# Kernel optimization log

Measured on AMD Instinct MI355X. Metric: run time of the kernel, lower is better.

## Reference

```python
import jax, jax.numpy as jnp
import numpy as np

N, E = 50000, 800000
C_IN, C_OUT, HID = 64, 64, 64


def setup_inputs() -> dict:
    key = jax.random.key(0)
    ks = jax.random.split(key, 12)
    def rn(k, shape, scale=0.05):
        return jax.random.normal(k, shape, dtype=jnp.float32) * scale
    return dict(
        x=jax.random.normal(ks[0], (N, C_IN), dtype=jnp.float32),
        pos=jax.random.normal(ks[1], (N, 3), dtype=jnp.float32),
        edge_index=jax.random.randint(ks[2], (2, E), 0, N),
        W_in=rn(ks[3], (C_IN, C_IN)), b_in=jnp.zeros((C_IN,), jnp.float32),
        W_out=rn(ks[4], (C_OUT, C_OUT)), b_out=jnp.zeros((C_OUT,), jnp.float32),
        W_lin=rn(ks[5], (C_OUT, C_IN)),   # PointTransformerConv.lin (value), bias=False
        W_src=rn(ks[6], (C_OUT, C_IN)),   # lin_src, bias=False
        W_dst=rn(ks[7], (C_OUT, C_IN)),   # lin_dst, bias=False
        pos_w1=rn(ks[8], (HID, 3)), pos_b1=jnp.zeros((HID,), jnp.float32),
        pos_w2=rn(ks[9], (C_OUT, HID)), pos_b2=jnp.zeros((C_OUT,), jnp.float32),
        att_w1=rn(ks[10], (HID, C_OUT)), att_b1=jnp.zeros((HID,), jnp.float32),
        att_w2=rn(ks[11], (C_OUT, HID)), att_b2=jnp.zeros((C_OUT,), jnp.float32),
    )


def _mlp2(y, w1, b1, w2, b2):
    # MLP([a, 64, b], batch_norm=False): Linear->ReLU->Linear->ReLU
    y = jax.nn.relu(y @ w1.T + b1)
    return jax.nn.relu(y @ w2.T + b2)


def reference(x, pos, edge_index, W_in, b_in, W_out, b_out, W_lin, W_src, W_dst,
              pos_w1, pos_b1, pos_w2, pos_b2, att_w1, att_b1, att_w2, att_b2):
    n = x.shape[0]
    h = jax.nn.relu(x @ W_in.T + b_in)            # lin_in + relu, (N, C_in)
    v = h @ W_lin.T                                # value projection (N, C_out)
    k_src = h @ W_src.T                            # alpha_j source part
    q_dst = h @ W_dst.T                            # alpha_i dest part
    # PointTransformerConv adds self-loops by default
    loop = jnp.arange(n)
    src = jnp.concatenate([edge_index[0], loop])   # (E+N,)
    dst = jnp.concatenate([edge_index[1], loop])
    # per-edge positional encoding: pos_nn(pos_i - pos_j)
    delta = _mlp2(pos[dst] - pos[src], pos_w1, pos_b1, pos_w2, pos_b2)
    # per-edge attention logits: attn_nn(alpha_i - alpha_j), (E+N, C_out)
    alpha = _mlp2(q_dst[dst] - k_src[src], att_w1, att_b1, att_w2, att_b2)
    # per-destination-node channelwise softmax (self-loops ensure no empty segment)
    amax = jax.ops.segment_max(alpha, dst, num_segments=n)
    ex = jnp.exp(alpha - amax[dst])
    denom = jax.ops.segment_sum(ex, dst, num_segments=n)
    w = ex / (denom[dst] + 1e-16)
    # message = alpha * (x_j + delta); aggregate = sum over neighbors
    out = jax.ops.segment_sum(w * (v[src] + delta), dst, num_segments=n)
    return jax.nn.relu(out @ W_out.T + b_out)
```

## Files before the change

### kernel.cpp

```cpp
#include <hip/hip_runtime.h>
#include <math.h>

#define NN 50000
#define EE 800000
#define ET (EE + NN)
#define C  64
#define NBLK 49
#define NCHUNK 831
#define ZBLK 463

typedef __attribute__((ext_vector_type(8))) _Float16 f16x8;
typedef __attribute__((ext_vector_type(4))) _Float16 f16x4;
typedef __attribute__((ext_vector_type(2))) _Float16 f16x2;
typedef __attribute__((ext_vector_type(4))) float f32x4;

__device__ __forceinline__ f16x2 pk2(float a, float b) {
  return __builtin_bit_cast(f16x2, __builtin_amdgcn_cvt_pkrtz(a, b));
}
__device__ __forceinline__ f16x4 pk4(float a, float b, float c, float d) {
  return __builtin_shufflevector(pk2(a, b), pk2(c, d), 0, 1, 2, 3);
}
__device__ __forceinline__ f16x8 pk8(const float* y) {
  const f16x4 lo = pk4(y[0], y[1], y[2], y[3]);
  const f16x4 hi = pk4(y[4], y[5], y[6], y[7]);
  return __builtin_shufflevector(lo, hi, 0, 1, 2, 3, 4, 5, 6, 7);
}

__device__ __forceinline__ f16x8 frag_ldh(const _Float16* base, int row,
                                          int kofs) {
  return *(const f16x8*)(base + row * 72 + kofs);
}

__device__ __forceinline__ void stage_w(_Float16* __restrict__ dst,
                                        const _Float16* __restrict__ src16,
                                        int tid) {
  const f16x8* src = (const f16x8*)(src16 + tid * 16);
  _Float16* d = dst + (tid >> 2) * 72 + (tid & 3) * 16;
  ((f16x8*)d)[0] = src[0];
  ((f16x8*)d)[1] = src[1];
}

__device__ __forceinline__ int psl(int e, int o) {
  return (e + 2 * o + (o >> 5)) & 63;
}

__global__ __launch_bounds__(256) void prep_kernel(
    const float* __restrict__ W_in, const float* __restrict__ W_lin,
    const float* __restrict__ W_src, const float* __restrict__ W_dst,
    const float* __restrict__ att_w1, const float* __restrict__ att_w2,
    const float* __restrict__ pos_w2, const float* __restrict__ W_out,
    _Float16* __restrict__ w16, int* __restrict__ cnt2) {
  const float* Ws[8] = {W_in, W_lin, W_src, W_dst, att_w1, att_w2, pos_w2, W_out};
  const float* src = Ws[blockIdx.x];
  _Float16* dst = w16 + blockIdx.x * 4096;
#pragma unroll
  for (int i = threadIdx.x * 4; i < 4096; i += 1024) {
    const float4 w = *(const float4*)(src + i);
    *(f16x4*)(dst + i) = pk4(w.x, w.y, w.z, w.w);
  }
  int4* cz = (int4*)(cnt2 + blockIdx.x * NN);
#pragma unroll 1
  for (int i = threadIdx.x; i < NN / 4; i += 256) cz[i] = make_int4(0, 0, 0, 0);
}

__global__ __launch_bounds__(256) void scan_partial(const int* __restrict__ cnt2,
                                                    int* __restrict__ bsum,
                                                    float* __restrict__ zeroreg) {
  const int t = threadIdx.x;
  if (blockIdx.x >= NBLK) {
    const int zb = blockIdx.x - NBLK;
    float4* dst = (float4*)zeroreg;
    const int total4 = 2 * NN * 64 / 4;
    const float4 z = make_float4(0.f, 0.f, 0.f, 0.f);
#pragma unroll 1
    for (int i = zb * 256 + t; i < total4; i += ZBLK * 256) dst[i] = z;
    return;
  }
  __shared__ int ws[4];
  const int base = blockIdx.x * 1024 + t * 4;
  int s = 0;
  if (base + 3 < NN) {
#pragma unroll
    for (int sh = 0; sh < 8; ++sh) {
      const int4 v = *(const int4*)(cnt2 + sh * NN + base);
      s += v.x + v.y + v.z + v.w;
    }
  } else {
#pragma unroll
    for (int i = 0; i < 4; ++i)
      if (base + i < NN)
#pragma unroll
        for (int sh = 0; sh < 8; ++sh) s += cnt2[sh * NN + base + i];
  }
#pragma unroll
  for (int off = 32; off; off >>= 1) s += __shfl_down(s, off, 64);
  if ((t & 63) == 0) ws[t >> 6] = s;
  __syncthreads();
  if (t == 0) bsum[blockIdx.x] = ws[0] + ws[1] + ws[2] + ws[3];
}

__global__ __launch_bounds__(256) void scan_final(const int* __restrict__ cnt2,
                                                  const int* __restrict__ bsum,
                                                  int* __restrict__ curs2) {
  __shared__ int tsum[256];
  __shared__ int sblk[64];
  const int t = threadIdx.x;
  if (t < 64) {
    const int mine = (t < NBLK) ? bsum[t] : 0;
    int v = mine;
#pragma unroll
    for (int off = 1; off < 64; off <<= 1) {
      const int u = __shfl_up(v, off, 64);
      if (t >= off) v += u;
    }
    sblk[t] = v - mine;
  }
  const int base = blockIdx.x * 1024 + t * 4;
  int c2[8][4];
  int v[4] = {0, 0, 0, 0};
  if (base + 3 < NN) {
#pragma unroll
    for (int sh = 0; sh < 8; ++sh) {
      const int4 x = *(const int4*)(cnt2 + sh * NN + base);
      c2[sh][0] = x.x; c2[sh][1] = x.y; c2[sh][2] = x.z; c2[sh][3] = x.w;
      v[0] += x.x; v[1] += x.y; v[2] += x.z; v[3] += x.w;
    }
  } else {
#pragma unroll
    for (int sh = 0; sh < 8; ++sh)
#pragma unroll
      for (int i = 0; i < 4; ++i) {
        const int c = (base + i < NN) ? cnt2[sh * NN + base + i] : 0;
        c2[sh][i] = c;
        v[i] += c;
      }
  }
  const int s = v[0] + v[1] + v[2] + v[3];
  tsum[t] = s;
  __syncthreads();
  for (int off = 1; off < 256; off <<= 1) {
    const int u = (t >= off) ? tsum[t - off] : 0;
    __syncthreads();
    tsum[t] += u;
    __syncthreads();
  }
  int ex = sblk[blockIdx.x] + tsum[t] - s;
  int offs[8][4];
#pragma unroll
  for (int i = 0; i < 4; ++i) {
    int run = ex;
#pragma unroll
    for (int sh = 0; sh < 8; ++sh) {
      offs[sh][i] = run;
      run += c2[sh][i];
    }
    ex += v[i];
  }
  if (base + 3 < NN) {
#pragma unroll
    for (int sh = 0; sh < 8; ++sh)
      *(int4*)(curs2 + sh * NN + base) =
          make_int4(offs[sh][0], offs[sh][1], offs[sh][2], offs[sh][3]);
  } else {
#pragma unroll
    for (int sh = 0; sh < 8; ++sh)
#pragma unroll
      for (int i = 0; i < 4; ++i)
        if (base + i < NN) curs2[sh * NN + base + i] = offs[sh][i];
  }
}

__global__ __launch_bounds__(256) void scatter_kernel(const int* __restrict__ ei,
                                                      int* __restrict__ curs2,
                                                      int2* __restrict__ srt) {
  const int chunk = blockIdx.x;
  int* cs = curs2 + (chunk & 7) * NN;
  const int e0 = chunk * 1024 + threadIdx.x * 4;
  if (e0 >= ET) return;
  int s[4], d[4];
  if (e0 + 3 < EE) {
    const int4 sv = *(const int4*)(ei + e0);
    const int4 dv = *(const int4*)(ei + EE + e0);
    s[0] = sv.x; s[1] = sv.y; s[2] = sv.z; s[3] = sv.w;
    d[0] = dv.x; d[1] = dv.y; d[2] = dv.z; d[3] = dv.w;
  } else {
#pragma unroll
    for (int i = 0; i < 4; ++i) {
      const int e = e0 + i;
      if (e < EE) {
        s[i] = ei[e];
        d[i] = ei[EE + e];
      } else if (e < ET) {
        s[i] = d[i] = e - EE;
      } else {
        s[i] = d[i] = -1;
      }
    }
  }
#pragma unroll
  for (int i = 0; i < 4; ++i) {
    if (d[i] >= 0) {
      const int p = atomicAdd(&cs[d[i]], 1);
      srt[p] = make_int2(s[i], d[i]);
    }
  }
}

__global__ __launch_bounds__(256, 3) void node_proj(
    const float* __restrict__ x, const float* __restrict__ b_in,
    const _Float16* __restrict__ w16, const int* __restrict__ ei,
    int* __restrict__ cnt2, _Float16* __restrict__ vh,
    _Float16* __restrict__ kh, _Float16* __restrict__ qh) {
  __shared__ __align__(16) _Float16 wlds[4 * 4608];
  __shared__ __align__(16) _Float16 hlds[4608];
  __shared__ float biasv[64];

  const int tid = threadIdx.x;
  const int nb = blockIdx.x * 64;
  const int l15 = tid & 15;
  const int quad = (tid >> 4) & 3;
  const int wband = tid >> 6;
  const int nloc = wband * 16 + l15;
  const int gn = nb + nloc;

#pragma unroll 1
  for (int chunk = blockIdx.x; chunk < NCHUNK; chunk += gridDim.x) {
    int* cs = cnt2 + (chunk & 7) * NN;
    const int e0 = chunk * 1024 + tid * 4;
    if (e0 < ET) {
      int d[4];
      if (e0 + 3 < EE) {
        const int4 dv = *(const int4*)(ei + EE + e0);
        d[0] = dv.x; d[1] = dv.y; d[2] = dv.z; d[3] = dv.w;
      } else {
#pragma unroll
        for (int i = 0; i < 4; ++i) {
          const int e = e0 + i;
          d[i] = (e < EE) ? ei[EE + e] : ((e < ET) ? e - EE : -1);
        }
      }
#pragma unroll
      for (int i = 0; i < 4; ++i)
        if (d[i] >= 0) atomicAdd(&cs[d[i]], 1);
    }
  }

#pragma unroll
  for (int w = 0; w < 4; ++w) stage_w(wlds + w * 4608, w16 + w * 4096, tid);
  if (tid < 64) biasv[tid] = b_in[tid];

  f16x8 bfrag[2];
#pragma unroll
  for (int ks = 0; ks < 2; ++ks) {
    float y[8] = {0.f, 0.f, 0.f, 0.f, 0.f, 0.f, 0.f, 0.f};
    if (gn < NN) {
      const float4 a = *(const float4*)(x + (size_t)gn * 64 + ks * 32 + quad * 8);
      const float4 b = *(const float4*)(x + (size_t)gn * 64 + ks * 32 + quad * 8 + 4);
      y[0] = a.x; y[1] = a.y; y[2] = a.z; y[3] = a.w;
      y[4] = b.x; y[5] = b.y; y[6] = b.z; y[7] = b.w;
    }
    bfrag[ks] = pk8(y);
  }
  __syncthreads();

#pragma unroll
  for (int t = 0; t < 4; ++t) {
    f32x4 acc = {0.f, 0.f, 0.f, 0.f};
#pragma unroll
    for (int ks = 0; ks < 2; ++ks) {
      const f16x8 af = frag_ldh(wlds, t * 16 + l15, ks * 32 + quad * 8);
      acc = __builtin_amdgcn_mfma_f32_16x16x32_f16(af, bfrag[ks], acc, 0, 0, 0);
    }
    const int hb = t * 16 + quad * 4;
    *(f16x4*)(hlds + nloc * 72 + hb) =
        pk4(fmaxf(acc[0] + biasv[hb + 0], 0.f), fmaxf(acc[1] + biasv[hb + 1], 0.f),
            fmaxf(acc[2] + biasv[hb + 2], 0.f), fmaxf(acc[3] + biasv[hb + 3], 0.f));
  }
  __syncthreads();

  f16x8 hfrag[2];
#pragma unroll
  for (int ks = 0; ks < 2; ++ks)
    hfrag[ks] = frag_ldh(hlds, nloc, ks * 32 + quad * 8);

  _Float16* outs[3] = {vh, kh, qh};
#pragma unroll
  for (int p = 0; p < 3; ++p) {
    const _Float16* W = wlds + (p + 1) * 4608;
#pragma unroll
    for (int t = 0; t < 4; ++t) {
      f32x4 acc = {0.f, 0.f, 0.f, 0.f};
#pragma unroll
      for (int ks = 0; ks < 2; ++ks) {
        const f16x8 af = frag_ldh(W, t * 16 + l15, ks * 32 + quad * 8);
        acc = __builtin_amdgcn_mfma_f32_16x16x32_f16(af, hfrag[ks], acc, 0, 0, 0);
      }
      if (gn < NN) {
        *(f16x4*)(outs[p] + (size_t)gn * 64 + t * 16 + quad * 4) =
            pk4(acc[0], acc[1], acc[2], acc[3]);
      }
    }
  }
}

__global__ __launch_bounds__(256, 5) void edge_pass(
    const int2* __restrict__ srt, const float* __restrict__ pos,
    const _Float16* __restrict__ vh, const _Float16* __restrict__ kh,
    const _Float16* __restrict__ qh, const _Float16* __restrict__ w16,
    const float* __restrict__ att_b1, const float* __restrict__ att_b2,
    const float* __restrict__ pos_w1, const float* __restrict__ pos_b1,
    const float* __restrict__ pos_b2, float* __restrict__ num,
    float* __restrict__ den) {
  __shared__ __align__(16) _Float16 smem[13824];
  __shared__ __align__(16) float posw1T[3 * 64];
  __shared__ float b1s[64], b2s[64], pb1s[64], pb2s[64];
  __shared__ int dsts[64];

  _Float16* W1 = smem;
  _Float16* W2 = smem + 4608;
  _Float16* HP = smem + 9216;
  f16x2* pairb = (f16x2*)smem;

  const int tid = threadIdx.x;
  const int eb = blockIdx.x * 64;
  const int l15 = tid & 15;
  const int quad = (tid >> 4) & 3;
  const int wband = tid >> 6;
  const int eloc = wband * 16 + l15;

  int s_mine, d_mine;
  f16x8 bfrag[2];
  float dp0, dp1, dp2;
  {
    const int e = eb + eloc;
    int2 sd = make_int2(0, 0);
    int valid_d = -1;
    if (e < ET) {
      sd = srt[e];
      valid_d = sd.y;
    }
    s_mine = sd.x;
    d_mine = sd.y;
    if (quad == 0) dsts[eloc] = valid_d;
#pragma unroll
    for (int ks = 0; ks < 2; ++ks) {
      const f16x8 qv =
          *(const f16x8*)(qh + (size_t)d_mine * 64 + ks * 32 + quad * 8);
      const f16x8 kv =
          *(const f16x8*)(kh + (size_t)s_mine * 64 + ks * 32 + quad * 8);
      bfrag[ks] = qv - kv;
    }
    dp0 = pos[(size_t)d_mine * 3 + 0] - pos[(size_t)s_mine * 3 + 0];
    dp1 = pos[(size_t)d_mine * 3 + 1] - pos[(size_t)s_mine * 3 + 1];
    dp2 = pos[(size_t)d_mine * 3 + 2] - pos[(size_t)s_mine * 3 + 2];
  }

  stage_w(W1, w16 + 4 * 4096, tid);
  stage_w(W2, w16 + 5 * 4096, tid);
  if (tid < 64) {
    b1s[tid] = att_b1[tid];
    b2s[tid] = att_b2[tid];
    pb1s[tid] = pos_b1[tid];
    pb2s[tid] = pos_b2[tid];
    posw1T[0 * 64 + tid] = pos_w1[tid * 3 + 0];
    posw1T[1 * 64 + tid] = pos_w1[tid * 3 + 1];
    posw1T[2 * 64 + tid] = pos_w1[tid * 3 + 2];
  }
  __syncthreads();

#pragma unroll
  for (int t = 0; t < 4; ++t) {
    f32x4 acc = {0.f, 0.f, 0.f, 0.f};
#pragma unroll
    for (int ks = 0; ks < 2; ++ks) {
      const f16x8 af = frag_ldh(W1, t * 16 + l15, ks * 32 + quad * 8);
      acc = __builtin_amdgcn_mfma_f32_16x16x32_f16(af, bfrag[ks], acc, 0, 0, 0);
    }
    const int hb = t * 16 + quad * 4;
    *(f16x4*)(HP + eloc * 72 + hb) =
        pk4(fmaxf(acc[0] + b1s[hb + 0], 0.f), fmaxf(acc[1] + b1s[hb + 1], 0.f),
            fmaxf(acc[2] + b1s[hb + 2], 0.f), fmaxf(acc[3] + b1s[hb + 3], 0.f));
  }

  f16x8 hpfrag[2];
#pragma unroll
  for (int ks = 0; ks < 2; ++ks) {
    float hv[8];
#pragma unroll
    for (int j = 0; j < 8; ++j) {
      const int i = ks * 32 + quad * 8 + j;
      float h = pb1s[i];
      h = fmaf(dp0, posw1T[i], h);
      h = fmaf(dp1, posw1T[64 + i], h);
      h = fmaf(dp2, posw1T[128 + i], h);
      hv[j] = fmaxf(h, 0.f);
    }
    hpfrag[ks] = pk8(hv);
  }

  float ex[16];
  {
    f16x8 hfrag[2];
#pragma unroll
    for (int ks = 0; ks < 2; ++ks)
      hfrag[ks] = frag_ldh(HP, eloc, ks * 32 + quad * 8);
#pragma unroll
    for (int t = 0; t < 4; ++t) {
      f32x4 acc = {0.f, 0.f, 0.f, 0.f};
#pragma unroll
      for (int ks = 0; ks < 2; ++ks) {
        const f16x8 af = frag_ldh(W2, t * 16 + l15, ks * 32 + quad * 8);
        acc = __builtin_amdgcn_mfma_f32_16x16x32_f16(af, hfrag[ks], acc, 0, 0, 0);
      }
      const int ob = t * 16 + quad * 4;
#pragma unroll
      for (int r = 0; r < 4; ++r)
        ex[t * 4 + r] = __expf(fmaxf(acc[r] + b2s[ob + r], 0.f));
    }
  }
  float vr[16];
#pragma unroll
  for (int t = 0; t < 4; ++t) {
    const f16x4 v4 = *(const f16x4*)(vh + (size_t)s_mine * 64 + t * 16 + quad * 4);
    vr[t * 4 + 0] = (float)v4[0];
    vr[t * 4 + 1] = (float)v4[1];
    vr[t * 4 + 2] = (float)v4[2];
    vr[t * 4 + 3] = (float)v4[3];
  }
  __syncthreads();

  stage_w(HP, w16 + 6 * 4096, tid);
  __syncthreads();

  float del[16];
#pragma unroll
  for (int t = 0; t < 4; ++t) {
    f32x4 acc = {0.f, 0.f, 0.f, 0.f};
#pragma unroll
    for (int ks = 0; ks < 2; ++ks) {
      const f16x8 af = frag_ldh(HP, t * 16 + l15, ks * 32 + quad * 8);
      acc = __builtin_amdgcn_mfma_f32_16x16x32_f16(af, hpfrag[ks], acc, 0, 0, 0);
    }
    const int ob = t * 16 + quad * 4;
#pragma unroll
    for (int r = 0; r < 4; ++r)
      del[t * 4 + r] = fmaxf(acc[r] + pb2s[ob + r], 0.f);
  }

#pragma unroll
  for (int t = 0; t < 4; ++t) {
#pragma unroll
    for (int r = 0; r < 4; ++r) {
      const int o = t * 16 + quad * 4 + r;
      const float e_ = ex[t * 4 + r];
      pairb[o * 64 + psl(eloc, o)] =
          pk2(e_ * (vr[t * 4 + r] + del[t * 4 + r]), e_);
    }
  }
  __syncthreads();

  {
    const int c = tid & 63;
    const int r = tid >> 6;
    float am = 0.f, ae = 0.f;
    int cur = -1;
#pragma unroll 1
    for (int t2 = 0; t2 < 16; ++t2) {
      const int el = r * 16 + t2;
      const int d = dsts[el];
      if (d != cur) {
        if (cur >= 0) {
          unsafeAtomicAdd(num + (size_t)cur * 64 + c, am);
          unsafeAtomicAdd(den + (size_t)cur * 64 + c, ae);
        }
        cur = d;
        am = 0.f;
        ae = 0.f;
      }
      if (d >= 0) {
        const f16x2 pe = pairb[c * 64 + psl(el, c)];
        am += (float)pe[0];
        ae += (float)pe[1];
      }
    }
    if (cur >= 0) {
      unsafeAtomicAdd(num + (size_t)cur * 64 + c, am);
      unsafeAtomicAdd(den + (size_t)cur * 64 + c, ae);
    }
  }
}

__global__ __launch_bounds__(256, 4) void out_proj(
    const float* __restrict__ num, const float* __restrict__ den,
    const _Float16* __restrict__ w16, const float* __restrict__ b_out,
    float* __restrict__ out) {
  __shared__ __align__(16) _Float16 wlds[4608];
  __shared__ float biasv[64];

  const int tid = threadIdx.x;
  const int nb = blockIdx.x * 64;
  const int l15 = tid & 15;
  const int quad = (tid >> 4) & 3;
  const int wband = tid >> 6;
  const int gn = nb + wband * 16 + l15;

  stage_w(wlds, w16 + 7 * 4096, tid);
  if (tid < 64) biasv[tid] = b_out[tid];

  f16x8 bfrag[2];
#pragma unroll
  for (int ks = 0; ks < 2; ++ks) {
    float y[8] = {0.f, 0.f, 0.f, 0.f, 0.f, 0.f, 0.f, 0.f};
    if (gn < NN) {
      const size_t base = (size_t)gn * 64 + ks * 32 + quad * 8;
      const float4 n0 = *(const float4*)(num + base);
      const float4 n1 = *(const float4*)(num + base + 4);
      const float4 d0 = *(const float4*)(den + base);
      const float4 d1 = *(const float4*)(den + base + 4);
      y[0] = n0.x / (d0.x + 1e-16f); y[1] = n0.y / (d0.y + 1e-16f);
      y[2] = n0.z / (d0.z + 1e-16f); y[3] = n0.w / (d0.w + 1e-16f);
      y[4] = n1.x / (d1.x + 1e-16f); y[5] = n1.y / (d1.y + 1e-16f);
      y[6] = n1.z / (d1.z + 1e-16f); y[7] = n1.w / (d1.w + 1e-16f);
    }
    bfrag[ks] = pk8(y);
  }
  __syncthreads();

#pragma unroll
  for (int t = 0; t < 4; ++t) {
    f32x4 acc = {0.f, 0.f, 0.f, 0.f};
#pragma unroll
    for (int ks = 0; ks < 2; ++ks) {
      const f16x8 af = frag_ldh(wlds, t * 16 + l15, ks * 32 + quad * 8);
      acc = __builtin_amdgcn_mfma_f32_16x16x32_f16(af, bfrag[ks], acc, 0, 0, 0);
    }
    if (gn < NN) {
      const int ob = t * 16 + quad * 4;
      float4 r;
      r.x = fmaxf(acc[0] + biasv[ob + 0], 0.f);
      r.y = fmaxf(acc[1] + biasv[ob + 1], 0.f);
      r.z = fmaxf(acc[2] + biasv[ob + 2], 0.f);
      r.w = fmaxf(acc[3] + biasv[ob + 3], 0.f);
      *(float4*)(out + (size_t)gn * 64 + ob) = r;
    }
  }
}

extern "C" void kernel_launch(void* const* d_in, const int* in_sizes, int n_in,
                              void* d_out, int out_size, void* d_ws,
                              size_t ws_size, hipStream_t stream) {
  const float* x      = (const float*)d_in[0];
  const float* pos    = (const float*)d_in[1];
  const int*   ei     = (const int*)d_in[2];
  const float* W_in   = (const float*)d_in[3];
  const float* b_in   = (const float*)d_in[4];
  const float* W_out  = (const float*)d_in[5];
  const float* b_out  = (const float*)d_in[6];
  const float* W_lin  = (const float*)d_in[7];
  const float* W_src  = (const float*)d_in[8];
  const float* W_dst  = (const float*)d_in[9];
  const float* pos_w1 = (const float*)d_in[10];
  const float* pos_b1 = (const float*)d_in[11];
  const float* pos_w2 = (const float*)d_in[12];
  const float* pos_b2 = (const float*)d_in[13];
  const float* att_w1 = (const float*)d_in[14];
  const float* att_b1 = (const float*)d_in[15];
  const float* att_w2 = (const float*)d_in[16];
  const float* att_b2 = (const float*)d_in[17];

  float* ws = (float*)d_ws;
  const size_t NC = (size_t)NN * C;
  float* num = ws;
  float* den = ws + NC;
  _Float16* vh = (_Float16*)(ws + 2 * NC);
  _Float16* kh = vh + NC;
  _Float16* qh = kh + NC;
  _Float16* w16 = qh + NC;
  int* ib     = (int*)(w16 + 8 * 4096);
  int* cnt2   = ib;
  int* curs2  = ib + 8 * NN;
  int* bsum   = ib + 16 * NN;
  int2* srt   = (int2*)(((uintptr_t)(bsum + NBLK) + 15) & ~(uintptr_t)15);

  const dim3 blk(256);
  prep_kernel<<<dim3(8), blk, 0, stream>>>(W_in, W_lin, W_src, W_dst, att_w1,
                                           att_w2, pos_w2, W_out, w16, cnt2);
  node_proj<<<dim3((NN + 63) / 64), blk, 0, stream>>>(x, b_in, w16, ei, cnt2,
                                                      vh, kh, qh);
  scan_partial<<<dim3(NBLK + ZBLK), blk, 0, stream>>>(cnt2, bsum, num);
  scan_final<<<dim3(NBLK), blk, 0, stream>>>(cnt2, bsum, curs2);
  scatter_kernel<<<dim3(NCHUNK), blk, 0, stream>>>(ei, curs2, srt);
  edge_pass<<<dim3((ET + 63) / 64), blk, 0, stream>>>(
      srt, pos, vh, kh, qh, w16, att_b1, att_b2, pos_w1, pos_b1, pos_b2, num,
      den);
  out_proj<<<dim3((NN + 63) / 64), blk, 0, stream>>>(num, den, w16, b_out,
                                                     (float*)d_out);
}
```

Measured before the change: 300.5 us.

## Reduce per-destination edge segments with MFMA selection matrices instead of scalar loops

The per-block segmented reduction of (weighted message, exp) pairs now runs as MFMA matrix multiplies against a 0/1 selection matrix. That matrix is built from a ballot over destination-run boundaries and handles up to 8 runs per pass, then each run is written with atomic adds. The softmax exponent switches to exp2, with log2(e) folded into the fp16 att_w2 weights and the att_b2 bias. The prep kernel is widened to 64 blocks for zeroing the count buffer. The cost is extra LDS staging and syncs, and a loop whose trip count depends on how many runs a block has. The fp16 rounding of the scaled weights changes numerics slightly.

```diff
diff --git a/kernel.cpp b/kernel.cpp
--- a/kernel.cpp
+++ b/kernel.cpp
@@ -40,27 +40,28 @@
   ((f16x8*)d)[1] = src[1];
 }
 
-__device__ __forceinline__ int psl(int e, int o) {
-  return (e + 2 * o + (o >> 5)) & 63;
-}
-
 __global__ __launch_bounds__(256) void prep_kernel(
     const float* __restrict__ W_in, const float* __restrict__ W_lin,
     const float* __restrict__ W_src, const float* __restrict__ W_dst,
     const float* __restrict__ att_w1, const float* __restrict__ att_w2,
     const float* __restrict__ pos_w2, const float* __restrict__ W_out,
     _Float16* __restrict__ w16, int* __restrict__ cnt2) {
-  const float* Ws[8] = {W_in, W_lin, W_src, W_dst, att_w1, att_w2, pos_w2, W_out};
-  const float* src = Ws[blockIdx.x];
-  _Float16* dst = w16 + blockIdx.x * 4096;
-#pragma unroll
-  for (int i = threadIdx.x * 4; i < 4096; i += 1024) {
-    const float4 w = *(const float4*)(src + i);
-    *(f16x4*)(dst + i) = pk4(w.x, w.y, w.z, w.w);
-  }
-  int4* cz = (int4*)(cnt2 + blockIdx.x * NN);
+  if (blockIdx.x < 8) {
+    const float* Ws[8] = {W_in, W_lin, W_src, W_dst, att_w1, att_w2, pos_w2,
+                          W_out};
+    const float* src = Ws[blockIdx.x];
+    _Float16* dst = w16 + blockIdx.x * 4096;
+    const float sc = (blockIdx.x == 5) ? 1.44269504088896340736f : 1.0f;
+#pragma unroll
+    for (int i = threadIdx.x * 4; i < 4096; i += 1024) {
+      const float4 w = *(const float4*)(src + i);
+      *(f16x4*)(dst + i) = pk4(w.x * sc, w.y * sc, w.z * sc, w.w * sc);
+    }
+  }
+  int4* cz = (int4*)cnt2;
 #pragma unroll 1
-  for (int i = threadIdx.x; i < NN / 4; i += 256) cz[i] = make_int4(0, 0, 0, 0);
+  for (int i = blockIdx.x * 256 + threadIdx.x; i < 2 * NN; i += 64 * 256)
+    cz[i] = make_int4(0, 0, 0, 0);
 }
 
 __global__ __launch_bounds__(256) void scan_partial(const int* __restrict__ cnt2,
@@ -315,17 +316,20 @@
   __shared__ __align__(16) float posw1T[3 * 64];
   __shared__ float b1s[64], b2s[64], pb1s[64], pb2s[64];
   __shared__ int dsts[64];
+  __shared__ int dstu[64];
 
   _Float16* W1 = smem;
   _Float16* W2 = smem + 4608;
   _Float16* HP = smem + 9216;
-  f16x2* pairb = (f16x2*)smem;
+  _Float16* PAIR = smem;
+  _Float16* ST = smem + 9216;
 
   const int tid = threadIdx.x;
   const int eb = blockIdx.x * 64;
   const int l15 = tid & 15;
   const int quad = (tid >> 4) & 3;
   const int wband = tid >> 6;
+  const int lane = tid & 63;
   const int eloc = wband * 16 + l15;
 
   int s_mine, d_mine;
@@ -359,7 +363,7 @@
   stage_w(W2, w16 + 5 * 4096, tid);
   if (tid < 64) {
     b1s[tid] = att_b1[tid];
-    b2s[tid] = att_b2[tid];
+    b2s[tid] = att_b2[tid] * 1.44269504088896340736f;
     pb1s[tid] = pos_b1[tid];
     pb2s[tid] = pos_b2[tid];
     posw1T[0 * 64 + tid] = pos_w1[tid * 3 + 0];
@@ -367,6 +371,17 @@
     posw1T[2 * 64 + tid] = pos_w1[tid * 3 + 2];
   }
   __syncthreads();
+
+  int rid_self, R, dball;
+  {
+    dball = dsts[lane];
+    const int dprev = dsts[(lane > 0) ? (lane - 1) : 0];
+    const bool flag = (dball >= 0) && (lane == 0 || dball != dprev);
+    const unsigned long long m = __ballot(flag);
+    R = (int)__popcll(m);
+    rid_self = (int)__popcll(m & ((2ull << lane) - 1)) - 1;
+    if (wband == 0 && flag) dstu[rid_self] = dball;
+  }
 
 #pragma unroll
   for (int t = 0; t < 4; ++t) {
@@ -415,7 +430,7 @@
       const int ob = t * 16 + quad * 4;
 #pragma unroll
       for (int r = 0; r < 4; ++r)
-        ex[t * 4 + r] = __expf(fmaxf(acc[r] + b2s[ob + r], 0.f));
+        ex[t * 4 + r] = __builtin_exp2f(fmaxf(acc[r] + b2s[ob + r], 0.f));
     }
   }
   float vr[16];
@@ -453,40 +468,57 @@
     for (int r = 0; r < 4; ++r) {
       const int o = t * 16 + quad * 4 + r;
       const float e_ = ex[t * 4 + r];
-      pairb[o * 64 + psl(eloc, o)] =
+      *(f16x2*)(PAIR + o * 136 + eloc * 2) =
           pk2(e_ * (vr[t * 4 + r] + del[t * 4 + r]), e_);
     }
   }
   __syncthreads();
 
-  {
-    const int c = tid & 63;
-    const int r = tid >> 6;
-    float am = 0.f, ae = 0.f;
-    int cur = -1;
+  if (wband == 0) {
+    const f16x8 z = {0, 0, 0, 0, 0, 0, 0, 0};
 #pragma unroll 1
-    for (int t2 = 0; t2 < 16; ++t2) {
-      const int el = r * 16 + t2;
-      const int d = dsts[el];
-      if (d != cur) {
-        if (cur >= 0) {
-          unsafeAtomicAdd(num + (size_t)cur * 64 + c, am);
-          unsafeAtomicAdd(den + (size_t)cur * 64 + c, ae);
-        }
-        cur = d;
-        am = 0.f;
-        ae = 0.f;
+    for (int i = lane; i < 272; i += 64) ((f16x8*)ST)[i] = z;
+    if (dball >= 0 && rid_self < 8) {
+      ST[(2 * rid_self + 0) * 136 + 2 * lane + 0] = (_Float16)1.0f;
+      ST[(2 * rid_self + 1) * 136 + 2 * lane + 1] = (_Float16)1.0f;
+    }
+  }
+  __syncthreads();
+
+  const int chq = wband * 16 + quad * 4;
+  const int jrun = l15 >> 1;
+  float* const base_np = (l15 & 1) ? den : num;
+#pragma unroll 1
+  for (int rt = 0;; ++rt) {
+    f32x4 racc = {0.f, 0.f, 0.f, 0.f};
+#pragma unroll
+    for (int ks = 0; ks < 4; ++ks) {
+      const f16x8 af =
+          *(const f16x8*)(PAIR + (wband * 16 + l15) * 136 + ks * 32 + quad * 8);
+      const f16x8 bf = *(const f16x8*)(ST + l15 * 136 + ks * 32 + quad * 8);
+      racc = __builtin_amdgcn_mfma_f32_16x16x32_f16(af, bf, racc, 0, 0, 0);
+    }
+    const int run = rt * 8 + jrun;
+    if (run < R) {
+      float* p = base_np + (size_t)dstu[run] * 64 + chq;
+      unsafeAtomicAdd(p + 0, racc[0]);
+      unsafeAtomicAdd(p + 1, racc[1]);
+      unsafeAtomicAdd(p + 2, racc[2]);
+      unsafeAtomicAdd(p + 3, racc[3]);
+    }
+    if ((rt + 1) * 8 >= R) break;
+    __syncthreads();
+    if (wband == 0) {
+      const f16x8 z = {0, 0, 0, 0, 0, 0, 0, 0};
+#pragma unroll 1
+      for (int i = lane; i < 272; i += 64) ((f16x8*)ST)[i] = z;
+      const int lr = rid_self - (rt + 1) * 8;
+      if (dball >= 0 && lr >= 0 && lr < 8) {
+        ST[(2 * lr + 0) * 136 + 2 * lane + 0] = (_Float16)1.0f;
+        ST[(2 * lr + 1) * 136 + 2 * lane + 1] = (_Float16)1.0f;
       }
-      if (d >= 0) {
-        const f16x2 pe = pairb[c * 64 + psl(el, c)];
-        am += (float)pe[0];
-        ae += (float)pe[1];
-      }
-    }
-    if (cur >= 0) {
-      unsafeAtomicAdd(num + (size_t)cur * 64 + c, am);
-      unsafeAtomicAdd(den + (size_t)cur * 64 + c, ae);
-    }
+    }
+    __syncthreads();
   }
 }
 
@@ -583,8 +615,8 @@
   int2* srt   = (int2*)(((uintptr_t)(bsum + NBLK) + 15) & ~(uintptr_t)15);
 
   const dim3 blk(256);
-  prep_kernel<<<dim3(8), blk, 0, stream>>>(W_in, W_lin, W_src, W_dst, att_w1,
-                                           att_w2, pos_w2, W_out, w16, cnt2);
+  prep_kernel<<<dim3(64), blk, 0, stream>>>(W_in, W_lin, W_src, W_dst, att_w1,
+                                            att_w2, pos_w2, W_out, w16, cnt2);
   node_proj<<<dim3((NN + 63) / 64), blk, 0, stream>>>(x, b_in, w16, ei, cnt2,
                                                       vh, kh, qh);
   scan_partial<<<dim3(NBLK + ZBLK), blk, 0, stream>>>(cnt2, bsum, num);
```

Result: slower. 337.1 us (+12.2%).

## Swizzle edge-pass LDS weight tiles, use exp2 with folded log2e, widen prep grid

Applied to the files above, without the earlier changes.

The padded 72-stride LDS layout for the attention and positional MLP weights and the hidden tile is replaced by an unpadded 128-byte-row XOR swizzle. This cuts shared memory per block so occupancy can go from 5 to 6 blocks per CU while still avoiding bank conflicts. log2(e) is folded into att_w2 during prep and into att_b2 at load, so the softmax uses exp2 instead of expf; since ReLU commutes with a positive scale this gives the same result. The prep kernel now runs on 64 blocks instead of 8 to spread out zeroing the count arrays. The risk is higher register pressure from the tighter launch bound.

```diff
diff --git a/kernel.cpp b/kernel.cpp
--- a/kernel.cpp
+++ b/kernel.cpp
@@ -30,7 +30,6 @@
                                           int kofs) {
   return *(const f16x8*)(base + row * 72 + kofs);
 }
-
 __device__ __forceinline__ void stage_w(_Float16* __restrict__ dst,
                                         const _Float16* __restrict__ src16,
                                         int tid) {
@@ -40,6 +39,23 @@
   ((f16x8*)d)[1] = src[1];
 }
 
+__device__ __forceinline__ int swzb(int row, int colbyte) {
+  return row * 128 + (colbyte ^ ((row & 7) << 4));
+}
+__device__ __forceinline__ f16x8 frag_lds(const _Float16* base, int row,
+                                          int kofs) {
+  return *(const f16x8*)((const char*)base + swzb(row, kofs * 2));
+}
+__device__ __forceinline__ void stage_ws(_Float16* __restrict__ dst,
+                                         const _Float16* __restrict__ src16,
+                                         int tid) {
+  const f16x8* src = (const f16x8*)(src16 + tid * 16);
+  const int row = tid >> 2;
+  const int c0 = (tid & 3) * 32;
+  *(f16x8*)((char*)dst + swzb(row, c0)) = src[0];
+  *(f16x8*)((char*)dst + swzb(row, c0 + 16)) = src[1];
+}
+
 __device__ __forceinline__ int psl(int e, int o) {
   return (e + 2 * o + (o >> 5)) & 63;
 }
@@ -50,17 +66,22 @@
     const float* __restrict__ att_w1, const float* __restrict__ att_w2,
     const float* __restrict__ pos_w2, const float* __restrict__ W_out,
     _Float16* __restrict__ w16, int* __restrict__ cnt2) {
-  const float* Ws[8] = {W_in, W_lin, W_src, W_dst, att_w1, att_w2, pos_w2, W_out};
-  const float* src = Ws[blockIdx.x];
-  _Float16* dst = w16 + blockIdx.x * 4096;
-#pragma unroll
-  for (int i = threadIdx.x * 4; i < 4096; i += 1024) {
-    const float4 w = *(const float4*)(src + i);
-    *(f16x4*)(dst + i) = pk4(w.x, w.y, w.z, w.w);
-  }
-  int4* cz = (int4*)(cnt2 + blockIdx.x * NN);
+  if (blockIdx.x < 8) {
+    const float* Ws[8] = {W_in, W_lin, W_src, W_dst, att_w1, att_w2, pos_w2,
+                          W_out};
+    const float* src = Ws[blockIdx.x];
+    _Float16* dst = w16 + blockIdx.x * 4096;
+    const float sc = (blockIdx.x == 5) ? 1.44269504088896340736f : 1.0f;
+#pragma unroll
+    for (int i = threadIdx.x * 4; i < 4096; i += 1024) {
+      const float4 w = *(const float4*)(src + i);
+      *(f16x4*)(dst + i) = pk4(w.x * sc, w.y * sc, w.z * sc, w.w * sc);
+    }
+  }
+  int4* cz = (int4*)cnt2;
 #pragma unroll 1
-  for (int i = threadIdx.x; i < NN / 4; i += 256) cz[i] = make_int4(0, 0, 0, 0);
+  for (int i = blockIdx.x * 256 + threadIdx.x; i < 2 * NN; i += 64 * 256)
+    cz[i] = make_int4(0, 0, 0, 0);
 }
 
 __global__ __launch_bounds__(256) void scan_partial(const int* __restrict__ cnt2,
@@ -303,7 +324,7 @@
   }
 }
 
-__global__ __launch_bounds__(256, 5) void edge_pass(
+__global__ __launch_bounds__(256, 6) void edge_pass(
     const int2* __restrict__ srt, const float* __restrict__ pos,
     const _Float16* __restrict__ vh, const _Float16* __restrict__ kh,
     const _Float16* __restrict__ qh, const _Float16* __restrict__ w16,
@@ -311,14 +332,14 @@
     const float* __restrict__ pos_w1, const float* __restrict__ pos_b1,
     const float* __restrict__ pos_b2, float* __restrict__ num,
     float* __restrict__ den) {
-  __shared__ __align__(16) _Float16 smem[13824];
+  __shared__ __align__(16) _Float16 smem[12288];
   __shared__ __align__(16) float posw1T[3 * 64];
   __shared__ float b1s[64], b2s[64], pb1s[64], pb2s[64];
   __shared__ int dsts[64];
 
   _Float16* W1 = smem;
-  _Float16* W2 = smem + 4608;
-  _Float16* HP = smem + 9216;
+  _Float16* W2 = smem + 4096;
+  _Float16* HP = smem + 8192;
   f16x2* pairb = (f16x2*)smem;
 
   const int tid = threadIdx.x;
@@ -355,11 +376,11 @@
     dp2 = pos[(size_t)d_mine * 3 + 2] - pos[(size_t)s_mine * 3 + 2];
   }
 
-  stage_w(W1, w16 + 4 * 4096, tid);
-  stage_w(W2, w16 + 5 * 4096, tid);
+  stage_ws(W1, w16 + 4 * 4096, tid);
+  stage_ws(W2, w16 + 5 * 4096, tid);
   if (tid < 64) {
     b1s[tid] = att_b1[tid];
-    b2s[tid] = att_b2[tid];
+    b2s[tid] = att_b2[tid] * 1.44269504088896340736f;
     pb1s[tid] = pos_b1[tid];
     pb2s[tid] = pos_b2[tid];
     posw1T[0 * 64 + tid] = pos_w1[tid * 3 + 0];
@@ -373,11 +394,11 @@
     f32x4 acc = {0.f, 0.f, 0.f, 0.f};
 #pragma unroll
     for (int ks = 0; ks < 2; ++ks) {
-      const f16x8 af = frag_ldh(W1, t * 16 + l15, ks * 32 + quad * 8);
+      const f16x8 af = frag_lds(W1, t * 16 + l15, ks * 32 + quad * 8);
       acc = __builtin_amdgcn_mfma_f32_16x16x32_f16(af, bfrag[ks], acc, 0, 0, 0);
     }
     const int hb = t * 16 + quad * 4;
-    *(f16x4*)(HP + eloc * 72 + hb) =
+    *(f16x4*)((char*)HP + swzb(eloc, hb * 2)) =
         pk4(fmaxf(acc[0] + b1s[hb + 0], 0.f), fmaxf(acc[1] + b1s[hb + 1], 0.f),
             fmaxf(acc[2] + b1s[hb + 2], 0.f), fmaxf(acc[3] + b1s[hb + 3], 0.f));
   }
@@ -403,19 +424,19 @@
     f16x8 hfrag[2];
 #pragma unroll
     for (int ks = 0; ks < 2; ++ks)
-      hfrag[ks] = frag_ldh(HP, eloc, ks * 32 + quad * 8);
+      hfrag[ks] = frag_lds(HP, eloc, ks * 32 + quad * 8);
 #pragma unroll
     for (int t = 0; t < 4; ++t) {
       f32x4 acc = {0.f, 0.f, 0.f, 0.f};
 #pragma unroll
       for (int ks = 0; ks < 2; ++ks) {
-        const f16x8 af = frag_ldh(W2, t * 16 + l15, ks * 32 + quad * 8);
+        const f16x8 af = frag_lds(W2, t * 16 + l15, ks * 32 + quad * 8);
         acc = __builtin_amdgcn_mfma_f32_16x16x32_f16(af, hfrag[ks], acc, 0, 0, 0);
       }
       const int ob = t * 16 + quad * 4;
 #pragma unroll
       for (int r = 0; r < 4; ++r)
-        ex[t * 4 + r] = __expf(fmaxf(acc[r] + b2s[ob + r], 0.f));
+        ex[t * 4 + r] = __builtin_exp2f(fmaxf(acc[r] + b2s[ob + r], 0.f));
     }
   }
   float vr[16];
@@ -429,7 +450,7 @@
   }
   __syncthreads();
 
-  stage_w(HP, w16 + 6 * 4096, tid);
+  stage_ws(HP, w16 + 6 * 4096, tid);
   __syncthreads();
 
   float del[16];
@@ -438,7 +459,7 @@
     f32x4 acc = {0.f, 0.f, 0.f, 0.f};
 #pragma unroll
     for (int ks = 0; ks < 2; ++ks) {
-      const f16x8 af = frag_ldh(HP, t * 16 + l15, ks * 32 + quad * 8);
+      const f16x8 af = frag_lds(HP, t * 16 + l15, ks * 32 + quad * 8);
       acc = __builtin_amdgcn_mfma_f32_16x16x32_f16(af, hpfrag[ks], acc, 0, 0, 0);
     }
     const int ob = t * 16 + quad * 4;
@@ -583,8 +604,8 @@
   int2* srt   = (int2*)(((uintptr_t)(bsum + NBLK) + 15) & ~(uintptr_t)15);
 
   const dim3 blk(256);
-  prep_kernel<<<dim3(8), blk, 0, stream>>>(W_in, W_lin, W_src, W_dst, att_w1,
-                                           att_w2, pos_w2, W_out, w16, cnt2);
+  prep_kernel<<<dim3(64), blk, 0, stream>>>(W_in, W_lin, W_src, W_dst, att_w1,
+                                            att_w2, pos_w2, W_out, w16, cnt2);
   node_proj<<<dim3((NN + 63) / 64), blk, 0, stream>>>(x, b_in, w16, ei, cnt2,
                                                       vh, kh, qh);
   scan_partial<<<dim3(NBLK + ZBLK), blk, 0, stream>>>(cnt2, bsum, num);
```

Result: faster. 291.5 us (-3.0%).
